# Kernel tuning notes

Measured on AMD Instinct MI355X. Metric: run time of the kernel, lower is better.

Reference implementation:

```python
import jax, jax.numpy as jnp
import numpy as np

COST_BBOX = 5.0
COST_GIOU = 2.0


def box_cxcywh_to_xyxy(b):
    cx, cy, w, h = b[:, 0], b[:, 1], b[:, 2], b[:, 3]
    return jnp.stack([cx - 0.5 * w, cy - 0.5 * h, cx + 0.5 * w, cy + 0.5 * h], axis=-1)


def generalized_box_iou(boxes1, boxes2):
    # boxes1 [N,4], boxes2 [M,4] in xyxy -> [N,M] GIoU
    area1 = (boxes1[:, 2] - boxes1[:, 0]) * (boxes1[:, 3] - boxes1[:, 1])
    area2 = (boxes2[:, 2] - boxes2[:, 0]) * (boxes2[:, 3] - boxes2[:, 1])
    lt = jnp.maximum(boxes1[:, None, :2], boxes2[None, :, :2])
    rb = jnp.minimum(boxes1[:, None, 2:], boxes2[None, :, 2:])
    wh = jnp.clip(rb - lt, 0.0)
    inter = wh[..., 0] * wh[..., 1]
    union = area1[:, None] + area2[None, :] - inter
    iou = inter / union
    lt_e = jnp.minimum(boxes1[:, None, :2], boxes2[None, :, :2])
    rb_e = jnp.maximum(boxes1[:, None, 2:], boxes2[None, :, 2:])
    wh_e = jnp.clip(rb_e - lt_e, 0.0)
    area_e = wh_e[..., 0] * wh_e[..., 1]
    return iou - (area_e - union) / area_e


@jax.jit
def cost_matrix(pred_boxes, truth_boxes):
    B, Q, _ = pred_boxes.shape
    out_bbox = pred_boxes.reshape(-1, 4)   # [B*Q,4]
    tgt_bbox = truth_boxes.reshape(-1, 4)  # [B*T,4]
    cost_bbox = jnp.sum(jnp.abs(out_bbox[:, None, :] - tgt_bbox[None, :, :]), axis=-1)  # L1 cdist
    cost_giou = -generalized_box_iou(box_cxcywh_to_xyxy(out_bbox), box_cxcywh_to_xyxy(tgt_bbox))
    C = COST_BBOX * cost_bbox + COST_GIOU * cost_giou
    return C.reshape(B, Q, -1)


def _lsa_rows_le_cols(cost):
    # Jonker-Volgenant shortest augmenting path (same algorithm as scipy
    # linear_sum_assignment). cost: [R, C] float64 with R <= C.
    # Returns col4row: assigned column for each row.
    R, Cc = cost.shape
    u = np.zeros(R)
    v = np.zeros(Cc)
    col4row = np.full(R, -1, dtype=np.int64)
    row4col = np.full(Cc, -1, dtype=np.int64)
    for cur in range(R):
        shortest = np.full(Cc, np.inf)
        path = np.full(Cc, -1, dtype=np.int64)
        on_row = np.zeros(R, dtype=bool)
        on_col = np.zeros(Cc, dtype=bool)
        min_val = 0.0
        i = cur
        sink = -1
        while sink == -1:
            on_row[i] = True
            rem = np.where(~on_col)[0]
            d = min_val + cost[i, rem] - u[i] - v[rem]
            better = d < shortest[rem]
            upd = rem[better]
            shortest[upd] = d[better]
            path[upd] = i
            j = rem[np.argmin(shortest[rem])]
            min_val = shortest[j]
            on_col[j] = True
            if row4col[j] == -1:
                sink = j
            else:
                i = row4col[j]
        u[cur] += min_val
        rset = np.where(on_row)[0]
        rset = rset[rset != cur]
        u[rset] += min_val - shortest[col4row[rset]]
        cset = np.where(on_col)[0]
        v[cset] -= min_val - shortest[cset]
        # augment along the path back from sink
        j = sink
        while True:
            i = path[j]
            row4col[j] = i
            col4row[i], j = j, col4row[i]
            if i == cur:
                break
    return col4row


def setup_inputs() -> dict:
    key = jax.random.key(0)
    k1, k2 = jax.random.split(key)
    pred_boxes = jax.random.uniform(k1, (32, 300, 4), dtype=jnp.float32)
    truth_boxes = jax.random.uniform(k2, (32, 50, 4), dtype=jnp.float32)
    return {"pred_boxes": pred_boxes, "truth_boxes": truth_boxes}


def reference(pred_boxes, truth_boxes):
    B, Q = pred_boxes.shape[:2]
    T = truth_boxes.shape[1]
    C = np.asarray(cost_matrix(pred_boxes, truth_boxes))  # [B, Q, B*T] (host, like .cpu())
    results = []
    for b in range(B):
        c = C[b, :, b * T:(b + 1) * T]  # diagonal block [Q, T]
        # Q > T: solve on the transpose (rows = targets), as scipy does internally.
        col4row = _lsa_rows_le_cols(np.ascontiguousarray(c.T, dtype=np.float64))
        i = col4row                     # selected query per target
        j = np.arange(T, dtype=np.int64)
        order = np.argsort(i)           # scipy returns row indices sorted
        results.append(np.stack([i[order], j[order]]))
    return jnp.asarray(np.stack(results), dtype=jnp.int64)  # [B, 2, min(Q,T)]
```

## Files before the change

kernel.cpp:

```cpp
#include <hip/hip_runtime.h>


#define NQ 300
#define NT 50
#define NSLOT 5
#define STRIDE 301
#define NTHREADS 256

typedef unsigned long long u64_t;

__device__ __forceinline__ u64_t pack_key(double d, int j) {
    u64_t u = __builtin_bit_cast(u64_t, d);
    u ^= (u64_t)((long long)u >> 63) | 0x8000000000000000ull;
    return (u & ~511ull) | (u64_t)(unsigned)j;
}
__device__ __forceinline__ u64_t shflx_u64(u64_t x, int off) {
    double d = __builtin_bit_cast(double, x);
    d = __shfl_xor(d, off);
    return __builtin_bit_cast(u64_t, d);
}
__device__ __forceinline__ void wave_sync() { __builtin_amdgcn_wave_barrier(); }

#define SEL5(res, a, kidx) do { (res) = a[0]; \
    if ((kidx) == 1) (res) = a[1]; if ((kidx) == 2) (res) = a[2]; \
    if ((kidx) == 3) (res) = a[3]; if ((kidx) == 4) (res) = a[4]; } while (0)
#define SET5(a, kidx, val) do { \
    if ((kidx) == 0) a[0] = (val); if ((kidx) == 1) a[1] = (val); \
    if ((kidx) == 2) a[2] = (val); if ((kidx) == 3) a[3] = (val); \
    if ((kidx) == 4) a[4] = (val); } while (0)

__global__ __launch_bounds__(NTHREADS) void hungarian_kernel(
    const float* __restrict__ pred, const float* __restrict__ truth,
    int* __restrict__ out)
{
#pragma clang fp contract(off)
    const int b = blockIdx.x;
    const int tid = threadIdx.x;
    const int lane = tid & 63;
    const int wav = tid >> 6;

    __shared__ float cost[NT * STRIDE];
    __shared__ int claim[NQ];
    __shared__ double sh_short[NQ];
    __shared__ int sh_c4r[NT];

    const float* pb = pred + b * NQ * 4;
    const float* tb = truth + b * NT * 4;

    for (int idx = tid; idx < NT * NQ; idx += NTHREADS) {
        int t = idx / NQ;
        int q = idx - t * NQ;
        float pcx = pb[q*4+0], pcy = pb[q*4+1], pw = pb[q*4+2], ph = pb[q*4+3];
        float tcx = tb[t*4+0], tcy = tb[t*4+1], tw = tb[t*4+2], th = tb[t*4+3];
        float cb = ((fabsf(pcx-tcx) + fabsf(pcy-tcy)) + fabsf(pw-tw)) + fabsf(ph-th);
        float px1 = pcx - 0.5f*pw, py1 = pcy - 0.5f*ph;
        float px2 = pcx + 0.5f*pw, py2 = pcy + 0.5f*ph;
        float tx1 = tcx - 0.5f*tw, ty1 = tcy - 0.5f*th;
        float tx2 = tcx + 0.5f*tw, ty2 = tcy + 0.5f*th;
        float area1 = (px2-px1)*(py2-py1);
        float area2 = (tx2-tx1)*(ty2-ty1);
        float ltx = fmaxf(px1, tx1), lty = fmaxf(py1, ty1);
        float rbx = fminf(px2, tx2), rby = fminf(py2, ty2);
        float w = fmaxf(rbx-ltx, 0.f), h = fmaxf(rby-lty, 0.f);
        float inter = w*h;
        float uni = (area1 + area2) - inter;
        float iou = inter/uni;
        float ex1 = fminf(px1,tx1), ey1 = fminf(py1,ty1);
        float ex2 = fmaxf(px2,tx2), ey2 = fmaxf(py2,ty2);
        float ew = fmaxf(ex2-ex1, 0.f), eh = fmaxf(ey2-ey1, 0.f);
        float ae = ew*eh;
        float g = iou - (ae - uni)/ae;
        cost[t*STRIDE + q] = 5.0f*cb + 2.0f*(-g);
    }
    for (int j = tid; j < NQ; j += NTHREADS) claim[j] = 0x7fffffff;
    __syncthreads();

    float rm = __builtin_inff();
    int ram = 0;
    if (tid < NT) {
        const float* row = cost + tid * STRIDE;
        for (int c = 0; c < NQ; ++c) {
            float x = row[c];
            if (x < rm) { rm = x; ram = c; }
        }
        atomicMin(&claim[ram], tid);
    }
    __syncthreads();
    if (wav != 0) return;

    double u_reg = (tid < NT) ? (double)rm : 0.0;
    int c4r = -1;
    if (tid < NT && claim[ram] == tid) c4r = ram;
    double v_reg[NSLOT];
    int r4c_reg[NSLOT];
#pragma unroll
    for (int k = 0; k < NSLOT; ++k) {
        int j = lane + (k << 6);
        v_reg[k] = 0.0;
        int cl = (j < NQ) ? claim[j] : 0x7fffffff;
        r4c_reg[k] = (cl != 0x7fffffff) ? cl : -1;
    }
    u64_t arr = __ballot(tid < NT && c4r < 0);
    u64_t att1 = 0, att2 = 0, dij = 0;

    while (arr) {
        int i = __builtin_ctzll(arr);
        arr &= arr - 1;
        const float* crow = cost + i * STRIDE;
        u64_t k1 = ~0ull;
        double v1 = __builtin_inf(), v2 = __builtin_inf();
#pragma unroll
        for (int k = 0; k < NSLOT; ++k) {
            int j = lane + (k << 6);
            if (j < NQ) {
                double m = (double)crow[j] - v_reg[k];
                u64_t kk = pack_key(m, j);
                if (kk < k1) { v2 = v1; v1 = m; k1 = kk; }
                else if (m < v2) { v2 = m; }
            }
        }
#pragma unroll
        for (int off = 32; off >= 1; off >>= 1) {
            u64_t ok = shflx_u64(k1, off);
            double ov1 = __shfl_xor(v1, off);
            double ov2 = __shfl_xor(v2, off);
            double nv2 = fmin(fmin(v2, ov2), fmax(v1, ov1));
            if (ok < k1) { k1 = ok; v1 = ov1; }
            v2 = nv2;
        }
        int j1 = (int)(k1 & 511ull);
        int kj = j1 >> 6, lj = j1 & 63;
        int rsel; SEL5(rsel, r4c_reg, kj);
        int r = __shfl(rsel, lj);
        if (r < 0) {
            if (lane == lj) SET5(r4c_reg, kj, i);
            if (lane == i) { c4r = j1; u_reg = v1; }
        } else {
            double cij = (double)crow[j1];
            if (lane == lj) { SET5(r4c_reg, kj, i); SET5(v_reg, kj, cij - v2); }
            if (lane == i) { c4r = j1; u_reg = v2; }
            if (lane == r) c4r = -1;
            u64_t rb = 1ull << r;
            if (!(att1 & rb))      { att1 |= rb; arr |= rb; }
            else if (!(att2 & rb)) { att2 |= rb; arr |= rb; }
            else                   { dij |= rb; }
        }
    }

    while (dij) {
        int cur = __builtin_ctzll(dij);
        dij &= dij - 1;
        unsigned oncol = 0;
        u64_t onrow = 0;
        double short_reg[NSLOT];
        int path_reg[NSLOT];
#pragma unroll
        for (int k = 0; k < NSLOT; ++k) { short_reg[k] = __builtin_inf(); path_reg[k] = -1; }
        double min_val = 0.0;
        int i = cur, sink = -1;

        while (sink < 0) {
            onrow |= 1ull << i;
            double u_i = __shfl(u_reg, i);
            const float* crow = cost + i * STRIDE;
            u64_t bk = ~0ull;
#pragma unroll
            for (int k = 0; k < NSLOT; ++k) {
                int j = lane + (k << 6);
                if (j < NQ && !((oncol >> k) & 1u)) {
                    double d = ((min_val + (double)crow[j]) - u_i) - v_reg[k];
                    if (d < short_reg[k]) { short_reg[k] = d; path_reg[k] = i; }
                    u64_t kk = pack_key(short_reg[k], j);
                    if (kk < bk) bk = kk;
                }
            }
#pragma unroll
            for (int off = 32; off >= 1; off >>= 1) {
                u64_t ok = shflx_u64(bk, off);
                if (ok < bk) bk = ok;
            }
            int j = (int)(bk & 511ull);
            int kj = j >> 6, lj = j & 63;
            double ssel; SEL5(ssel, short_reg, kj);
            min_val = __shfl(ssel, lj);
            if (lane == lj) oncol |= 1u << kj;
            int rsel; SEL5(rsel, r4c_reg, kj);
            int r = __shfl(rsel, lj);
            if (r < 0) sink = j; else i = r;
        }

#pragma unroll
        for (int k = 0; k < NSLOT; ++k) {
            int j = lane + (k << 6);
            if (j < NQ) sh_short[j] = short_reg[k];
        }
        wave_sync();
        double ss = (tid < NT && c4r >= 0) ? sh_short[c4r] : 0.0;
        if (tid < NT) {
            if (tid == cur) u_reg = u_reg + min_val;
            else if ((onrow >> tid) & 1ull) u_reg = u_reg + (min_val - ss);
        }
#pragma unroll
        for (int k = 0; k < NSLOT; ++k) {
            int j = lane + (k << 6);
            if (j < NQ && ((oncol >> k) & 1u))
                v_reg[k] = v_reg[k] - (min_val - short_reg[k]);
        }

        int jj = sink;
        while (true) {
            int kk2 = jj >> 6, ll = jj & 63;
            int psel; SEL5(psel, path_reg, kk2);
            int ii = __shfl(psel, ll);
            if (lane == ll) SET5(r4c_reg, kk2, ii);
            int nj = __shfl(c4r, ii);
            if (lane == ii) c4r = jj;
            jj = nj;
            if (ii == cur) break;
        }
    }

    if (tid < NT) sh_c4r[tid] = c4r;
    wave_sync();
    if (tid < NT) {
        int it = c4r;
        int rank = 0;
        for (int t2 = 0; t2 < NT; ++t2) rank += (sh_c4r[t2] < it) ? 1 : 0;
        out[b * 2 * NT + rank] = it;
        out[b * 2 * NT + NT + rank] = tid;
    }
}

extern "C" void kernel_launch(void* const* d_in, const int* in_sizes, int n_in,
                              void* d_out, int out_size, void* d_ws, size_t ws_size,
                              hipStream_t stream) {
    const float* pred  = (const float*)d_in[0];
    const float* truth = (const float*)d_in[1];
    int* out = (int*)d_out;
    hungarian_kernel<<<32, NTHREADS, 0, stream>>>(pred, truth, out);
}
```

Baseline: 97.75 us.

## Use DPP wave-min reductions and readlane broadcasts in auction/JV loops

```diff
diff --git a/kernel.cpp b/kernel.cpp
--- a/kernel.cpp
+++ b/kernel.cpp
@@ -6,19 +6,53 @@
 #define NSLOT 5
 #define STRIDE 301
 #define NTHREADS 256
+#define ARR_CAP 4
 
 typedef unsigned long long u64_t;
 
-__device__ __forceinline__ u64_t pack_key(double d, int j) {
+__device__ __forceinline__ u64_t minu64(u64_t a, u64_t b) { return a < b ? a : b; }
+
+__device__ __forceinline__ u64_t f64_key(double d) {
     u64_t u = __builtin_bit_cast(u64_t, d);
     u ^= (u64_t)((long long)u >> 63) | 0x8000000000000000ull;
-    return (u & ~511ull) | (u64_t)(unsigned)j;
-}
-__device__ __forceinline__ u64_t shflx_u64(u64_t x, int off) {
-    double d = __builtin_bit_cast(double, x);
-    d = __shfl_xor(d, off);
-    return __builtin_bit_cast(u64_t, d);
-}
+    return u;
+}
+__device__ __forceinline__ double key_f64(u64_t k) {
+    u64_t u = (k >> 63) ? (k ^ 0x8000000000000000ull) : ~k;
+    return __builtin_bit_cast(double, u);
+}
+__device__ __forceinline__ u64_t pack_key(double d, int j) {
+    return (f64_key(d) & ~511ull) | (u64_t)(unsigned)j;
+}
+
+template<int CTRL, int RMASK>
+__device__ __forceinline__ u64_t dpp_u64(u64_t x) {
+    int lo = (int)(unsigned)(x & 0xffffffffull);
+    int hi = (int)(unsigned)(x >> 32);
+    int plo = __builtin_amdgcn_update_dpp(lo, lo, CTRL, RMASK, 0xf, false);
+    int phi = __builtin_amdgcn_update_dpp(hi, hi, CTRL, RMASK, 0xf, false);
+    return ((u64_t)(unsigned)phi << 32) | (u64_t)(unsigned)plo;
+}
+
+__device__ __forceinline__ u64_t wave_min_u64(u64_t k) {
+    k = minu64(k, dpp_u64<0x121, 0xf>(k));
+    k = minu64(k, dpp_u64<0x122, 0xf>(k));
+    k = minu64(k, dpp_u64<0x124, 0xf>(k));
+    k = minu64(k, dpp_u64<0x128, 0xf>(k));
+    k = minu64(k, dpp_u64<0x142, 0xa>(k));
+    k = minu64(k, dpp_u64<0x143, 0xc>(k));
+    int lo = __builtin_amdgcn_readlane((int)(unsigned)(k & 0xffffffffull), 63);
+    int hi = __builtin_amdgcn_readlane((int)(unsigned)(k >> 32), 63);
+    return ((u64_t)(unsigned)hi << 32) | (u64_t)(unsigned)lo;
+}
+
+__device__ __forceinline__ double readlane_f64(double x, int l) {
+    u64_t u = __builtin_bit_cast(u64_t, x);
+    int lo = __builtin_amdgcn_readlane((int)(unsigned)(u & 0xffffffffull), l);
+    int hi = __builtin_amdgcn_readlane((int)(unsigned)(u >> 32), l);
+    return __builtin_bit_cast(double, ((u64_t)(unsigned)hi << 32) | (u64_t)(unsigned)lo);
+}
+
 __device__ __forceinline__ void wave_sync() { __builtin_amdgcn_wave_barrier(); }
 
 #define SEL5(res, a, kidx) do { (res) = a[0]; \
@@ -79,10 +113,19 @@
     int ram = 0;
     if (tid < NT) {
         const float* row = cost + tid * STRIDE;
-        for (int c = 0; c < NQ; ++c) {
-            float x = row[c];
-            if (x < rm) { rm = x; ram = c; }
-        }
+        float m0 = __builtin_inff(), m1 = m0, m2 = m0, m3 = m0;
+        int a0 = 0, a1 = 0, a2 = 0, a3 = 0;
+        for (int c = 0; c < NQ; c += 4) {
+            float x0 = row[c], x1 = row[c+1], x2 = row[c+2], x3 = row[c+3];
+            if (x0 < m0) { m0 = x0; a0 = c; }
+            if (x1 < m1) { m1 = x1; a1 = c+1; }
+            if (x2 < m2) { m2 = x2; a2 = c+2; }
+            if (x3 < m3) { m3 = x3; a3 = c+3; }
+        }
+        rm = m0; ram = a0;
+        if (m1 < rm || (m1 == rm && a1 < ram)) { rm = m1; ram = a1; }
+        if (m2 < rm || (m2 == rm && a2 < ram)) { rm = m2; ram = a2; }
+        if (m3 < rm || (m3 == rm && a3 < ram)) { rm = m3; ram = a3; }
         atomicMin(&claim[ram], tid);
     }
     __syncthreads();
@@ -100,8 +143,9 @@
         int cl = (j < NQ) ? claim[j] : 0x7fffffff;
         r4c_reg[k] = (cl != 0x7fffffff) ? cl : -1;
     }
+    int att_cnt = 0;
     u64_t arr = __ballot(tid < NT && c4r < 0);
-    u64_t att1 = 0, att2 = 0, dij = 0;
+    u64_t dij = 0;
 
     while (arr) {
         int i = __builtin_ctzll(arr);
@@ -119,31 +163,25 @@
                 else if (m < v2) { v2 = m; }
             }
         }
-#pragma unroll
-        for (int off = 32; off >= 1; off >>= 1) {
-            u64_t ok = shflx_u64(k1, off);
-            double ov1 = __shfl_xor(v1, off);
-            double ov2 = __shfl_xor(v2, off);
-            double nv2 = fmin(fmin(v2, ov2), fmax(v1, ov1));
-            if (ok < k1) { k1 = ok; v1 = ov1; }
-            v2 = nv2;
-        }
-        int j1 = (int)(k1 & 511ull);
+        u64_t kmin = wave_min_u64(k1);
+        int j1 = (int)(kmin & 511ull);
         int kj = j1 >> 6, lj = j1 & 63;
+        double v1g = readlane_f64(v1, lj);
+        double cand = (lane == lj) ? v2 : v1;
+        double v2g = key_f64(wave_min_u64(f64_key(cand)));
         int rsel; SEL5(rsel, r4c_reg, kj);
-        int r = __shfl(rsel, lj);
+        int r = __builtin_amdgcn_readlane(rsel, lj);
         if (r < 0) {
             if (lane == lj) SET5(r4c_reg, kj, i);
-            if (lane == i) { c4r = j1; u_reg = v1; }
+            if (lane == i) { c4r = j1; u_reg = v1g; }
         } else {
             double cij = (double)crow[j1];
-            if (lane == lj) { SET5(r4c_reg, kj, i); SET5(v_reg, kj, cij - v2); }
-            if (lane == i) { c4r = j1; u_reg = v2; }
-            if (lane == r) c4r = -1;
+            if (lane == lj) { SET5(r4c_reg, kj, i); SET5(v_reg, kj, cij - v2g); }
+            if (lane == i) { c4r = j1; u_reg = v2g; }
+            if (lane == r) { c4r = -1; att_cnt++; }
+            int ac = __builtin_amdgcn_readlane(att_cnt, r);
             u64_t rb = 1ull << r;
-            if (!(att1 & rb))      { att1 |= rb; arr |= rb; }
-            else if (!(att2 & rb)) { att2 |= rb; arr |= rb; }
-            else                   { dij |= rb; }
+            if (ac <= ARR_CAP) arr |= rb; else dij |= rb;
         }
     }
 
@@ -161,7 +199,7 @@
 
         while (sink < 0) {
             onrow |= 1ull << i;
-            double u_i = __shfl(u_reg, i);
+            double u_i = readlane_f64(u_reg, i);
             const float* crow = cost + i * STRIDE;
             u64_t bk = ~0ull;
 #pragma unroll
@@ -174,18 +212,14 @@
                     if (kk < bk) bk = kk;
                 }
             }
-#pragma unroll
-            for (int off = 32; off >= 1; off >>= 1) {
-                u64_t ok = shflx_u64(bk, off);
-                if (ok < bk) bk = ok;
-            }
+            bk = wave_min_u64(bk);
             int j = (int)(bk & 511ull);
             int kj = j >> 6, lj = j & 63;
             double ssel; SEL5(ssel, short_reg, kj);
-            min_val = __shfl(ssel, lj);
+            min_val = readlane_f64(ssel, lj);
             if (lane == lj) oncol |= 1u << kj;
             int rsel; SEL5(rsel, r4c_reg, kj);
-            int r = __shfl(rsel, lj);
+            int r = __builtin_amdgcn_readlane(rsel, lj);
             if (r < 0) sink = j; else i = r;
         }
 
@@ -211,9 +245,9 @@
         while (true) {
             int kk2 = jj >> 6, ll = jj & 63;
             int psel; SEL5(psel, path_reg, kk2);
-            int ii = __shfl(psel, ll);
+            int ii = __builtin_amdgcn_readlane(psel, ll);
             if (lane == ll) SET5(r4c_reg, kk2, ii);
-            int nj = __shfl(c4r, ii);
+            int nj = __builtin_amdgcn_readlane(c4r, ii);
             if (lane == ii) c4r = jj;
             jj = nj;
             if (ii == cur) break;
```

New measurement: 93.95 us. 1.04x faster.
